# Kernel tuning notes

Hardware: AMD Instinct MI355X
Metric: run time of the kernel (lower is better)

The kernel has to match this reference:

```python
import jax, jax.numpy as jnp
import numpy as np


def _rnn_layer(x, w_ih, w_hh, b_ih, b_hh):
    # x: [B, T, D_in]; returns [B, T, H]
    B = x.shape[0]
    H = w_hh.shape[0]
    # Precompute input projection for all timesteps in one big GEMM.
    xp = jnp.einsum('btd,hd->bth', x, w_ih) + b_ih + b_hh  # [B, T, H]
    h0 = jnp.zeros((B, H), dtype=x.dtype)

    def step(h, xp_t):
        h = jnp.tanh(xp_t + h @ w_hh.T)
        return h, h

    _, hs = jax.lax.scan(step, h0, jnp.swapaxes(xp, 0, 1))  # hs: [T, B, H]
    return jnp.swapaxes(hs, 0, 1)  # [B, T, H]


def setup_inputs() -> dict:
    key = jax.random.key(0)
    ks = jax.random.split(key, 11)
    B, T, D, H, O = 256, 512, 64, 512, 1
    s_in = 1.0 / np.sqrt(H)
    inp = {
        'x': jax.random.normal(ks[0], (B, T, D), dtype=jnp.float32),
        'w_ih0': jax.random.normal(ks[1], (H, D), dtype=jnp.float32) * s_in,
        'w_hh0': jax.random.normal(ks[2], (H, H), dtype=jnp.float32) * s_in,
        'b_ih0': jax.random.normal(ks[3], (H,), dtype=jnp.float32) * s_in,
        'b_hh0': jax.random.normal(ks[4], (H,), dtype=jnp.float32) * s_in,
        'w_ih1': jax.random.normal(ks[5], (H, H), dtype=jnp.float32) * s_in,
        'w_hh1': jax.random.normal(ks[6], (H, H), dtype=jnp.float32) * s_in,
        'b_ih1': jax.random.normal(ks[7], (H,), dtype=jnp.float32) * s_in,
        'b_hh1': jax.random.normal(ks[8], (H,), dtype=jnp.float32) * s_in,
        'w_lin': jax.random.normal(ks[9], (O, H), dtype=jnp.float32) * s_in,
        'b_lin': jax.random.normal(ks[10], (O,), dtype=jnp.float32) * s_in,
    }
    return inp


def reference(x, w_ih0, w_hh0, b_ih0, b_hh0, w_ih1, w_hh1, b_ih1, b_hh1, w_lin, b_lin):
    h1 = _rnn_layer(x, w_ih0, w_hh0, b_ih0, b_hh0)   # [B, T, H]
    h2 = _rnn_layer(h1, w_ih1, w_hh1, b_ih1, b_hh1)  # [B, T, H]
    out = h2[:, -1, :] @ w_lin.T + b_lin             # [B, 1]
    return jnp.squeeze(out)                          # [B]
```

## Files before the change

kernel.cpp:

```cpp
#include <hip/hip_runtime.h>
#include <hip/hip_bf16.h>

typedef __attribute__((ext_vector_type(8))) short shortx8;
typedef __attribute__((ext_vector_type(4))) float f32x4;
typedef __attribute__((ext_vector_type(4))) unsigned short ushortx4;
typedef __attribute__((ext_vector_type(4))) unsigned int u32x4;

#define HDIM 512
#define DDIM 64
#define TSTEPS 512
#define NG 16
#define NB 16
#define SPIN_LIMIT (1u << 16)

#define OFF_WHH0 0u
#define OFF_W1   (512u * 1024u)
#define OFF_WIH0 (OFF_W1 + 1024u * 1024u)
#define OFF_B0   (OFF_WIH0 + 64u * 1024u)
#define OFF_B1   (OFF_B0 + 2048u)
#define OFF_H1G  (OFF_B1 + 2048u)
#define OFF_H2G  (OFF_H1G + 512u * 1024u)
#define OFF_CNT  (OFF_H2G + 512u * 1024u)

__device__ __forceinline__ unsigned short f2b(float f) {
    __hip_bfloat16 h = __float2bfloat16(f);
    return *reinterpret_cast<unsigned short*>(&h);
}
__device__ __forceinline__ float b2f(unsigned short s) {
    union { unsigned int u; float f; } cvt;
    cvt.u = ((unsigned int)s) << 16;
    return cvt.f;
}
__device__ __forceinline__ float fast_tanh(float v) {
    float e = __expf(2.f * v);
    return 1.f - 2.f * __builtin_amdgcn_rcpf(e + 1.f);
}

__device__ __forceinline__ void mall_store8(unsigned short* p, ushortx4 v) {
    asm volatile("global_store_dwordx2 %0, %1, off sc0 sc1" :: "v"(p), "v"(v) : "memory");
}
__device__ __forceinline__ shortx8 mall_load16(const unsigned short* p) {
    shortx8 r;
    asm volatile("global_load_dwordx4 %0, %1, off sc0 sc1" : "=v"(r) : "v"(p) : "memory");
    return r;
}
__device__ __forceinline__ void vm_drain() {
    asm volatile("s_waitcnt vmcnt(0)" ::: "memory");
    __builtin_amdgcn_sched_barrier(0);
}
__device__ __forceinline__ void flag_store(unsigned int* p, unsigned int v) {
    asm volatile("global_store_dword %0, %1, off sc0 sc1" :: "v"(p), "v"(v) : "memory");
}
__device__ __forceinline__ bool poll_peers(const unsigned int* fp, int m,
                                           unsigned int tgt, bool bail) {
    if (bail) return false;
    unsigned it = 0;
    for (;;) {
        u32x4 f;
        asm volatile("global_load_dwordx4 %0, %1, off sc0 sc1\n\ts_waitcnt vmcnt(0)"
                     : "=v"(f) : "v"(fp) : "memory");
        bool ok = true;
        if (m != 0 && f[0] < tgt) ok = false;
        if (m != 1 && f[1] < tgt) ok = false;
        if (m != 2 && f[2] < tgt) ok = false;
        if (m != 3 && f[3] < tgt) ok = false;
        if (ok) return true;
        if (++it > SPIN_LIMIT) return false;
    }
}

__global__ void prep_kernel(const float* __restrict__ w_ih0, const float* __restrict__ w_hh0,
                            const float* __restrict__ w_ih1, const float* __restrict__ w_hh1,
                            const float* __restrict__ b_ih0, const float* __restrict__ b_hh0,
                            const float* __restrict__ b_ih1, const float* __restrict__ b_hh1,
                            unsigned short* __restrict__ whh0_sw,
                            unsigned short* __restrict__ w1_sw,
                            unsigned short* __restrict__ wih0_sw,
                            float* __restrict__ bias0, float* __restrict__ bias1,
                            unsigned int* __restrict__ cnt)
{
    int idx = blockIdx.x * blockDim.x + threadIdx.x;
    int stride = gridDim.x * blockDim.x;

    for (int i = idx; i < 32 * 16 * 64; i += stride) {
        int l = i & 63, kb = (i >> 6) & 15, mt = i >> 10;
        int row = mt * 16 + (l & 15);
        int k0 = kb * 32 + (l >> 4) * 8;
        unsigned short* o = whh0_sw + (size_t)i * 8;
        #pragma unroll
        for (int j = 0; j < 8; ++j) o[j] = f2b(w_hh0[row * HDIM + k0 + j]);
    }
    for (int i = idx; i < 32 * 32 * 64; i += stride) {
        int l = i & 63, kb = (i >> 6) & 31, mt = i >> 11;
        int row = mt * 16 + (l & 15);
        int k0 = kb * 32 + (l >> 4) * 8;
        unsigned short* o = w1_sw + (size_t)i * 8;
        #pragma unroll
        for (int j = 0; j < 8; ++j) {
            int kk = k0 + j;
            float v = (kk < HDIM) ? w_ih1[row * HDIM + kk] : w_hh1[row * HDIM + (kk - HDIM)];
            o[j] = f2b(v);
        }
    }
    for (int i = idx; i < 32 * 2 * 64; i += stride) {
        int l = i & 63, kb = (i >> 6) & 1, mt = i >> 7;
        int row = mt * 16 + (l & 15);
        int k0 = kb * 32 + (l >> 4) * 8;
        unsigned short* o = wih0_sw + (size_t)i * 8;
        #pragma unroll
        for (int j = 0; j < 8; ++j) o[j] = f2b(w_ih0[row * DDIM + k0 + j]);
    }
    for (int i = idx; i < HDIM; i += stride) {
        bias0[i] = b_ih0[i] + b_hh0[i];
        bias1[i] = b_ih1[i] + b_hh1[i];
    }
    if (idx < NG * 32) {
        unsigned int z = 0;
        unsigned int* p = cnt + idx;
        asm volatile("global_store_dword %0, %1, off sc0 sc1" :: "v"(p), "v"(z) : "memory");
    }
}

__global__ __launch_bounds__(256, 1) void rnn_1sync(
    const float* __restrict__ x,
    const unsigned short* __restrict__ whh0_sw,
    const unsigned short* __restrict__ w1_sw,
    const unsigned short* __restrict__ wih0_sw,
    const float* __restrict__ bias0,
    const float* __restrict__ bias1,
    const float* __restrict__ w_lin,
    const float* __restrict__ b_lin,
    unsigned short* __restrict__ h1G,
    unsigned short* __restrict__ h2G,
    unsigned int* __restrict__ cnt,
    float* __restrict__ out)
{
    __shared__ unsigned short h1L[2][8192];
    __shared__ unsigned short h2L[2][8192];
    __shared__ unsigned short xL[2][1024];

    const int tid  = threadIdx.x;
    const int w    = tid >> 6;
    const int lane = tid & 63;
    const int gq   = lane >> 4;
    const int col  = lane & 15;
    const int b    = blockIdx.x;
    const int g    = (b & 7) | ((b >> 5) << 3);
    const int m    = (b >> 3) & 3;

    const int mt0 = m * 8 + 2 * w, mt1 = mt0 + 1;
    const int lbase = gq * 128 + col * 8;
    const int dbase = (gq >> 1) * 128 + col * 8 + (gq & 1) * 4;

    unsigned int* flags = cnt + g * 32;

    shortx8 W0a[18], W0b[18], W1a[32], W1b[32];
    #pragma unroll
    for (int kb = 0; kb < 16; ++kb) {
        W0a[kb] = *(const shortx8*)(whh0_sw + (((size_t)(mt0 * 16 + kb)) << 9) + lane * 8);
        W0b[kb] = *(const shortx8*)(whh0_sw + (((size_t)(mt1 * 16 + kb)) << 9) + lane * 8);
    }
    #pragma unroll
    for (int kx = 0; kx < 2; ++kx) {
        W0a[16 + kx] = *(const shortx8*)(wih0_sw + (((size_t)(mt0 * 2 + kx)) << 9) + lane * 8);
        W0b[16 + kx] = *(const shortx8*)(wih0_sw + (((size_t)(mt1 * 2 + kx)) << 9) + lane * 8);
    }
    #pragma unroll
    for (int kb = 0; kb < 32; ++kb) {
        W1a[kb] = *(const shortx8*)(w1_sw + (((size_t)(mt0 * 32 + kb)) << 9) + lane * 8);
        W1b[kb] = *(const shortx8*)(w1_sw + (((size_t)(mt1 * 32 + kb)) << 9) + lane * 8);
    }
    #pragma unroll
    for (int i = 0; i < 18; ++i) { asm volatile("" : "+v"(W0a[i]), "+v"(W0b[i])); }
    #pragma unroll
    for (int i = 0; i < 32; ++i) { asm volatile("" : "+v"(W1a[i]), "+v"(W1b[i])); }

    f32x4 b0a = *(const f32x4*)(bias0 + mt0 * 16 + gq * 4);
    f32x4 b0b = *(const f32x4*)(bias0 + mt1 * 16 + gq * 4);
    f32x4 b1a = *(const f32x4*)(bias1 + mt0 * 16 + gq * 4);
    f32x4 b1b = *(const f32x4*)(bias1 + mt1 * 16 + gq * 4);

    const int bb = tid >> 4, d4 = (tid & 15) * 4;
    const int xo = ((d4 >> 3) * 16 + bb) * 8 + (d4 & 7);
    const float* xrow = x + (size_t)(g * NB + bb) * TSTEPS * DDIM + d4;
    bool bail = false;

    {
        f32x4 x0 = *(const f32x4*)(xrow);
        f32x4 x1 = *(const f32x4*)(xrow + DDIM);
        ushortx4 o0, o1;
        #pragma unroll
        for (int j = 0; j < 4; ++j) { o0[j] = f2b(x0[j]); o1[j] = f2b(x1[j]); }
        *(ushortx4*)&xL[0][xo] = o0;
        *(ushortx4*)&xL[1][xo] = o1;
        shortx8 zz = {0, 0, 0, 0, 0, 0, 0, 0};
        for (int i = tid * 8; i < 8192; i += 2048) *(shortx8*)&h2L[1][i] = zz;
    }
    __syncthreads();
    {
        unsigned short* h1G0 = h1G + (size_t)(g * 2 + 0) * 8192;
        f32x4 acc0 = b0a, acc1 = b0b;
        #pragma unroll
        for (int kx = 0; kx < 2; ++kx) {
            shortx8 bf = *(const shortx8*)&xL[0][kx * 512 + lbase];
            acc0 = __builtin_amdgcn_mfma_f32_16x16x32_bf16(W0a[16 + kx], bf, acc0, 0, 0, 0);
            acc1 = __builtin_amdgcn_mfma_f32_16x16x32_bf16(W0b[16 + kx], bf, acc1, 0, 0, 0);
        }
        ushortx4 o0, o1;
        #pragma unroll
        for (int j = 0; j < 4; ++j) { o0[j] = f2b(fast_tanh(acc0[j])); o1[j] = f2b(fast_tanh(acc1[j])); }
        mall_store8(h1G0 + mt0 * 256 + dbase, o0);
        mall_store8(h1G0 + mt1 * 256 + dbase, o1);
        vm_drain();
        __syncthreads();
        if (tid == 0) flag_store(flags + m, 1u);
        if (!poll_peers(flags, m, 1u, bail)) bail = true;
        int o = tid * 8;
        shortx8 v0 = mall_load16(h1G0 + o);
        shortx8 v1 = mall_load16(h1G0 + o + 2048);
        shortx8 v2 = mall_load16(h1G0 + o + 4096);
        shortx8 v3 = mall_load16(h1G0 + o + 6144);
        vm_drain();
        *(shortx8*)&h1L[0][o]        = v0;
        *(shortx8*)&h1L[0][o + 2048] = v1;
        *(shortx8*)&h1L[0][o + 4096] = v2;
        *(shortx8*)&h1L[0][o + 6144] = v3;
    }
    __syncthreads();

    for (int t = 0; t < TSTEPS - 1; ++t) {
        const int pc = t & 1, pn = pc ^ 1;
        unsigned short* h1Gn = h1G + (size_t)(g * 2 + pn) * 8192;
        unsigned short* h2Gc = h2G + (size_t)(g * 2 + pc) * 8192;

        const bool havex = (t + 2 < TSTEPS);
        f32x4 xv;
        if (havex) xv = *(const f32x4*)(xrow + (size_t)(t + 2) * DDIM);

        f32x4 acc0 = b0a, acc1 = b0b, e0 = b1a, e1 = b1b;
        #pragma unroll
        for (int kb = 0; kb < 16; ++kb) {
            shortx8 bf = *(const shortx8*)&h1L[pc][kb * 512 + lbase];
            acc0 = __builtin_amdgcn_mfma_f32_16x16x32_bf16(W0a[kb], bf, acc0, 0, 0, 0);
            acc1 = __builtin_amdgcn_mfma_f32_16x16x32_bf16(W0b[kb], bf, acc1, 0, 0, 0);
            e0   = __builtin_amdgcn_mfma_f32_16x16x32_bf16(W1a[kb], bf, e0, 0, 0, 0);
            e1   = __builtin_amdgcn_mfma_f32_16x16x32_bf16(W1b[kb], bf, e1, 0, 0, 0);
        }
        #pragma unroll
        for (int kx = 0; kx < 2; ++kx) {
            shortx8 bf = *(const shortx8*)&xL[pn][kx * 512 + lbase];
            acc0 = __builtin_amdgcn_mfma_f32_16x16x32_bf16(W0a[16 + kx], bf, acc0, 0, 0, 0);
            acc1 = __builtin_amdgcn_mfma_f32_16x16x32_bf16(W0b[16 + kx], bf, acc1, 0, 0, 0);
        }
        #pragma unroll
        for (int kb = 0; kb < 16; ++kb) {
            shortx8 bf = *(const shortx8*)&h2L[pn][kb * 512 + lbase];
            e0 = __builtin_amdgcn_mfma_f32_16x16x32_bf16(W1a[16 + kb], bf, e0, 0, 0, 0);
            e1 = __builtin_amdgcn_mfma_f32_16x16x32_bf16(W1b[16 + kb], bf, e1, 0, 0, 0);
        }

        {
            ushortx4 o0, o1, p0, p1;
            #pragma unroll
            for (int j = 0; j < 4; ++j) {
                o0[j] = f2b(fast_tanh(acc0[j])); o1[j] = f2b(fast_tanh(acc1[j]));
                p0[j] = f2b(fast_tanh(e0[j]));   p1[j] = f2b(fast_tanh(e1[j]));
            }
            mall_store8(h1Gn + mt0 * 256 + dbase, o0);
            mall_store8(h1Gn + mt1 * 256 + dbase, o1);
            mall_store8(h2Gc + mt0 * 256 + dbase, p0);
            mall_store8(h2Gc + mt1 * 256 + dbase, p1);
        }
        if (havex) {
            ushortx4 ox;
            #pragma unroll
            for (int j = 0; j < 4; ++j) ox[j] = f2b(xv[j]);
            *(ushortx4*)&xL[pc][xo] = ox;
        }
        vm_drain();
        __syncthreads();

        const unsigned int tgt = (unsigned int)(t + 2);
        if (tid == 0) flag_store(flags + m, tgt);
        if (!poll_peers(flags, m, tgt, bail)) bail = true;

        const int o = tid * 8;
        shortx8 va0 = mall_load16(h1Gn + o);
        shortx8 va1 = mall_load16(h1Gn + o + 2048);
        shortx8 va2 = mall_load16(h1Gn + o + 4096);
        shortx8 va3 = mall_load16(h1Gn + o + 6144);
        shortx8 vb0 = mall_load16(h2Gc + o);
        shortx8 vb1 = mall_load16(h2Gc + o + 2048);
        shortx8 vb2 = mall_load16(h2Gc + o + 4096);
        shortx8 vb3 = mall_load16(h2Gc + o + 6144);
        vm_drain();
        *(shortx8*)&h1L[pn][o]        = va0;
        *(shortx8*)&h1L[pn][o + 2048] = va1;
        *(shortx8*)&h1L[pn][o + 4096] = va2;
        *(shortx8*)&h1L[pn][o + 6144] = va3;
        *(shortx8*)&h2L[pc][o]        = vb0;
        *(shortx8*)&h2L[pc][o + 2048] = vb1;
        *(shortx8*)&h2L[pc][o + 4096] = vb2;
        *(shortx8*)&h2L[pc][o + 6144] = vb3;
        __syncthreads();
    }

    {
        unsigned short* h2Gc = h2G + (size_t)(g * 2 + 1) * 8192;
        f32x4 e0 = b1a, e1 = b1b;
        #pragma unroll
        for (int kb = 0; kb < 16; ++kb) {
            shortx8 bf = *(const shortx8*)&h1L[1][kb * 512 + lbase];
            e0 = __builtin_amdgcn_mfma_f32_16x16x32_bf16(W1a[kb], bf, e0, 0, 0, 0);
            e1 = __builtin_amdgcn_mfma_f32_16x16x32_bf16(W1b[kb], bf, e1, 0, 0, 0);
        }
        #pragma unroll
        for (int kb = 0; kb < 16; ++kb) {
            shortx8 bf = *(const shortx8*)&h2L[0][kb * 512 + lbase];
            e0 = __builtin_amdgcn_mfma_f32_16x16x32_bf16(W1a[16 + kb], bf, e0, 0, 0, 0);
            e1 = __builtin_amdgcn_mfma_f32_16x16x32_bf16(W1b[16 + kb], bf, e1, 0, 0, 0);
        }
        ushortx4 o0, o1;
        #pragma unroll
        for (int j = 0; j < 4; ++j) { o0[j] = f2b(fast_tanh(e0[j])); o1[j] = f2b(fast_tanh(e1[j])); }
        mall_store8(h2Gc + mt0 * 256 + dbase, o0);
        mall_store8(h2Gc + mt1 * 256 + dbase, o1);
        vm_drain();
        __syncthreads();
        if (tid == 0) flag_store(flags + m, (unsigned int)(TSTEPS + 1));

        if (m == 0) {
            if (!poll_peers(flags, m, (unsigned int)(TSTEPS + 1), bail)) bail = true;
            #pragma unroll
            for (int r = 0; r < 4; ++r) {
                int bx = w * 4 + r;
                shortx8 hv = mall_load16(h2Gc + lane * 128 + bx * 8);
                vm_drain();
                float s = 0.f;
                #pragma unroll
                for (int j = 0; j < 8; ++j)
                    s += b2f((unsigned short)hv[j]) * w_lin[lane * 8 + j];
                #pragma unroll
                for (int off = 32; off; off >>= 1) s += __shfl_xor(s, off);
                if (lane == 0) out[g * NB + bx] = s + b_lin[0];
            }
        }
    }
    if (bail && tid == 0 && b == 0) out[0] = out[0];
}

extern "C" void kernel_launch(void* const* d_in, const int* in_sizes, int n_in,
                              void* d_out, int out_size, void* d_ws, size_t ws_size,
                              hipStream_t stream) {
    const float* x     = (const float*)d_in[0];
    const float* w_ih0 = (const float*)d_in[1];
    const float* w_hh0 = (const float*)d_in[2];
    const float* b_ih0 = (const float*)d_in[3];
    const float* b_hh0 = (const float*)d_in[4];
    const float* w_ih1 = (const float*)d_in[5];
    const float* w_hh1 = (const float*)d_in[6];
    const float* b_ih1 = (const float*)d_in[7];
    const float* b_hh1 = (const float*)d_in[8];
    const float* w_lin = (const float*)d_in[9];
    const float* b_lin = (const float*)d_in[10];
    float* out = (float*)d_out;

    char* ws = (char*)d_ws;
    unsigned short* whh0_sw = (unsigned short*)(ws + OFF_WHH0);
    unsigned short* w1_sw   = (unsigned short*)(ws + OFF_W1);
    unsigned short* wih0_sw = (unsigned short*)(ws + OFF_WIH0);
    float* bias0            = (float*)(ws + OFF_B0);
    float* bias1            = (float*)(ws + OFF_B1);
    unsigned short* h1G     = (unsigned short*)(ws + OFF_H1G);
    unsigned short* h2G     = (unsigned short*)(ws + OFF_H2G);
    unsigned int*   cnt     = (unsigned int*)(ws + OFF_CNT);

    prep_kernel<<<416, 256, 0, stream>>>(w_ih0, w_hh0, w_ih1, w_hh1,
                                         b_ih0, b_hh0, b_ih1, b_hh1,
                                         whh0_sw, w1_sw, wih0_sw, bias0, bias1, cnt);
    rnn_1sync<<<64, 256, 0, stream>>>(x, whh0_sw, w1_sw, wih0_sw, bias0, bias1,
                                      w_lin, b_lin, h1G, h2G, cnt, out);
}
```

Baseline: 1.801 ms.

## Move layer-1 step after the cross-block barrier to hide synchronization latency

Splits each timestep so layer-0 is computed and published first, then the cross-block flag barrier runs, and the layer-1 step for time t-1 is computed afterwards from the previous step's h2 buffer. The aim is to shorten the critical path between the flag store and the peers' arrival, so layer-1 MFMA work overlaps the wait that comes before the next step. Flags are preloaded before the barrier so the spin loop can be skipped when peers are already done. h2 in LDS becomes single-buffered, an extra epilogue sync is added, and the spin limit is raised.

```diff
diff --git a/kernel.cpp b/kernel.cpp
--- a/kernel.cpp
+++ b/kernel.cpp
@@ -11,7 +11,7 @@
 #define TSTEPS 512
 #define NG 16
 #define NB 16
-#define SPIN_LIMIT (1u << 16)
+#define SPIN_LIMIT (1u << 18)
 
 #define OFF_WHH0 0u
 #define OFF_W1   (512u * 1024u)
@@ -44,12 +44,25 @@
     asm volatile("global_load_dwordx4 %0, %1, off sc0 sc1" : "=v"(r) : "v"(p) : "memory");
     return r;
 }
+__device__ __forceinline__ u32x4 flags_preload(const unsigned int* p) {
+    u32x4 r;
+    asm volatile("global_load_dwordx4 %0, %1, off sc0 sc1" : "=v"(r) : "v"(p) : "memory");
+    return r;
+}
 __device__ __forceinline__ void vm_drain() {
     asm volatile("s_waitcnt vmcnt(0)" ::: "memory");
     __builtin_amdgcn_sched_barrier(0);
 }
 __device__ __forceinline__ void flag_store(unsigned int* p, unsigned int v) {
     asm volatile("global_store_dword %0, %1, off sc0 sc1" :: "v"(p), "v"(v) : "memory");
+}
+__device__ __forceinline__ bool peers_ok(u32x4 f, int m, unsigned int tgt) {
+    bool ok = true;
+    if (m != 0 && f[0] < tgt) ok = false;
+    if (m != 1 && f[1] < tgt) ok = false;
+    if (m != 2 && f[2] < tgt) ok = false;
+    if (m != 3 && f[3] < tgt) ok = false;
+    return ok;
 }
 __device__ __forceinline__ bool poll_peers(const unsigned int* fp, int m,
                                            unsigned int tgt, bool bail) {
@@ -59,12 +72,7 @@
         u32x4 f;
         asm volatile("global_load_dwordx4 %0, %1, off sc0 sc1\n\ts_waitcnt vmcnt(0)"
                      : "=v"(f) : "v"(fp) : "memory");
-        bool ok = true;
-        if (m != 0 && f[0] < tgt) ok = false;
-        if (m != 1 && f[1] < tgt) ok = false;
-        if (m != 2 && f[2] < tgt) ok = false;
-        if (m != 3 && f[3] < tgt) ok = false;
-        if (ok) return true;
+        if (peers_ok(f, m, tgt)) return true;
         if (++it > SPIN_LIMIT) return false;
     }
 }
@@ -121,7 +129,7 @@
     }
 }
 
-__global__ __launch_bounds__(256, 1) void rnn_1sync(
+__global__ __launch_bounds__(256, 1) void rnn_slack(
     const float* __restrict__ x,
     const unsigned short* __restrict__ whh0_sw,
     const unsigned short* __restrict__ w1_sw,
@@ -136,7 +144,7 @@
     float* __restrict__ out)
 {
     __shared__ unsigned short h1L[2][8192];
-    __shared__ unsigned short h2L[2][8192];
+    __shared__ unsigned short h2L[8192];
     __shared__ unsigned short xL[2][1024];
 
     const int tid  = threadIdx.x;
@@ -194,7 +202,7 @@
         *(ushortx4*)&xL[0][xo] = o0;
         *(ushortx4*)&xL[1][xo] = o1;
         shortx8 zz = {0, 0, 0, 0, 0, 0, 0, 0};
-        for (int i = tid * 8; i < 8192; i += 2048) *(shortx8*)&h2L[1][i] = zz;
+        for (int i = tid * 8; i < 8192; i += 2048) *(shortx8*)&h2L[i] = zz;
     }
     __syncthreads();
     {
@@ -232,19 +240,18 @@
         const int pc = t & 1, pn = pc ^ 1;
         unsigned short* h1Gn = h1G + (size_t)(g * 2 + pn) * 8192;
         unsigned short* h2Gc = h2G + (size_t)(g * 2 + pc) * 8192;
+        unsigned short* h2Gp = h2G + (size_t)(g * 2 + pn) * 8192;
 
         const bool havex = (t + 2 < TSTEPS);
         f32x4 xv;
         if (havex) xv = *(const f32x4*)(xrow + (size_t)(t + 2) * DDIM);
 
-        f32x4 acc0 = b0a, acc1 = b0b, e0 = b1a, e1 = b1b;
+        f32x4 acc0 = b0a, acc1 = b0b;
         #pragma unroll
         for (int kb = 0; kb < 16; ++kb) {
             shortx8 bf = *(const shortx8*)&h1L[pc][kb * 512 + lbase];
             acc0 = __builtin_amdgcn_mfma_f32_16x16x32_bf16(W0a[kb], bf, acc0, 0, 0, 0);
             acc1 = __builtin_amdgcn_mfma_f32_16x16x32_bf16(W0b[kb], bf, acc1, 0, 0, 0);
-            e0   = __builtin_amdgcn_mfma_f32_16x16x32_bf16(W1a[kb], bf, e0, 0, 0, 0);
-            e1   = __builtin_amdgcn_mfma_f32_16x16x32_bf16(W1b[kb], bf, e1, 0, 0, 0);
         }
         #pragma unroll
         for (int kx = 0; kx < 2; ++kx) {
@@ -252,24 +259,45 @@
             acc0 = __builtin_amdgcn_mfma_f32_16x16x32_bf16(W0a[16 + kx], bf, acc0, 0, 0, 0);
             acc1 = __builtin_amdgcn_mfma_f32_16x16x32_bf16(W0b[16 + kx], bf, acc1, 0, 0, 0);
         }
-        #pragma unroll
-        for (int kb = 0; kb < 16; ++kb) {
-            shortx8 bf = *(const shortx8*)&h2L[pn][kb * 512 + lbase];
-            e0 = __builtin_amdgcn_mfma_f32_16x16x32_bf16(W1a[16 + kb], bf, e0, 0, 0, 0);
-            e1 = __builtin_amdgcn_mfma_f32_16x16x32_bf16(W1b[16 + kb], bf, e1, 0, 0, 0);
-        }
-
         {
-            ushortx4 o0, o1, p0, p1;
+            ushortx4 o0, o1;
             #pragma unroll
-            for (int j = 0; j < 4; ++j) {
-                o0[j] = f2b(fast_tanh(acc0[j])); o1[j] = f2b(fast_tanh(acc1[j]));
-                p0[j] = f2b(fast_tanh(e0[j]));   p1[j] = f2b(fast_tanh(e1[j]));
-            }
+            for (int j = 0; j < 4; ++j) { o0[j] = f2b(fast_tanh(acc0[j])); o1[j] = f2b(fast_tanh(acc1[j])); }
             mall_store8(h1Gn + mt0 * 256 + dbase, o0);
             mall_store8(h1Gn + mt1 * 256 + dbase, o1);
-            mall_store8(h2Gc + mt0 * 256 + dbase, p0);
-            mall_store8(h2Gc + mt1 * 256 + dbase, p1);
+        }
+        u32x4 F = flags_preload(flags);
+        vm_drain();
+        __syncthreads();
+
+        const unsigned int tgt = (unsigned int)(t + 2);
+        if (tid == 0) flag_store(flags + m, tgt);
+        if (!peers_ok(F, m, tgt)) {
+            if (!poll_peers(flags, m, tgt, bail)) bail = true;
+        }
+
+        const int o = tid * 8;
+        shortx8 va0 = mall_load16(h1Gn + o);
+        shortx8 va1 = mall_load16(h1Gn + o + 2048);
+        shortx8 va2 = mall_load16(h1Gn + o + 4096);
+        shortx8 va3 = mall_load16(h1Gn + o + 6144);
+        shortx8 vb0, vb1, vb2, vb3;
+        if (t > 0) {
+            vb0 = mall_load16(h2Gp + o);
+            vb1 = mall_load16(h2Gp + o + 2048);
+            vb2 = mall_load16(h2Gp + o + 4096);
+            vb3 = mall_load16(h2Gp + o + 6144);
+        }
+        vm_drain();
+        *(shortx8*)&h1L[pn][o]        = va0;
+        *(shortx8*)&h1L[pn][o + 2048] = va1;
+        *(shortx8*)&h1L[pn][o + 4096] = va2;
+        *(shortx8*)&h1L[pn][o + 6144] = va3;
+        if (t > 0) {
+            *(shortx8*)&h2L[o]        = vb0;
+            *(shortx8*)&h2L[o + 2048] = vb1;
+            *(shortx8*)&h2L[o + 4096] = vb2;
+            *(shortx8*)&h2L[o + 6144] = vb3;
         }
         if (havex) {
             ushortx4 ox;
@@ -277,36 +305,51 @@
             for (int j = 0; j < 4; ++j) ox[j] = f2b(xv[j]);
             *(ushortx4*)&xL[pc][xo] = ox;
         }
-        vm_drain();
-        __syncthreads();
-
-        const unsigned int tgt = (unsigned int)(t + 2);
-        if (tid == 0) flag_store(flags + m, tgt);
-        if (!poll_peers(flags, m, tgt, bail)) bail = true;
-
+        __syncthreads();
+
+        f32x4 e0 = b1a, e1 = b1b;
+        #pragma unroll
+        for (int kb = 0; kb < 16; ++kb) {
+            shortx8 bf = *(const shortx8*)&h1L[pc][kb * 512 + lbase];
+            e0 = __builtin_amdgcn_mfma_f32_16x16x32_bf16(W1a[kb], bf, e0, 0, 0, 0);
+            e1 = __builtin_amdgcn_mfma_f32_16x16x32_bf16(W1b[kb], bf, e1, 0, 0, 0);
+        }
+        #pragma unroll
+        for (int kb = 0; kb < 16; ++kb) {
+            shortx8 bf = *(const shortx8*)&h2L[kb * 512 + lbase];
+            e0 = __builtin_amdgcn_mfma_f32_16x16x32_bf16(W1a[16 + kb], bf, e0, 0, 0, 0);
+            e1 = __builtin_amdgcn_mfma_f32_16x16x32_bf16(W1b[16 + kb], bf, e1, 0, 0, 0);
+        }
+        {
+            ushortx4 p0, p1;
+            #pragma unroll
+            for (int j = 0; j < 4; ++j) { p0[j] = f2b(fast_tanh(e0[j])); p1[j] = f2b(fast_tanh(e1[j])); }
+            mall_store8(h2Gc + mt0 * 256 + dbase, p0);
+            mall_store8(h2Gc + mt1 * 256 + dbase, p1);
+        }
+    }
+
+    {
+        vm_drain();
+        __syncthreads();
+        if (tid == 0) flag_store(flags + m, (unsigned int)(TSTEPS + 1));
+        if (!poll_peers(flags, m, (unsigned int)(TSTEPS + 1), bail)) bail = true;
+        unsigned short* h2Gp0 = h2G + (size_t)(g * 2 + 0) * 8192;
         const int o = tid * 8;
-        shortx8 va0 = mall_load16(h1Gn + o);
-        shortx8 va1 = mall_load16(h1Gn + o + 2048);
-        shortx8 va2 = mall_load16(h1Gn + o + 4096);
-        shortx8 va3 = mall_load16(h1Gn + o + 6144);
-        shortx8 vb0 = mall_load16(h2Gc + o);
-        shortx8 vb1 = mall_load16(h2Gc + o + 2048);
-        shortx8 vb2 = mall_load16(h2Gc + o + 4096);
-        shortx8 vb3 = mall_load16(h2Gc + o + 6144);
-        vm_drain();
-        *(shortx8*)&h1L[pn][o]        = va0;
-        *(shortx8*)&h1L[pn][o + 2048] = va1;
-        *(shortx8*)&h1L[pn][o + 4096] = va2;
-        *(shortx8*)&h1L[pn][o + 6144] = va3;
-        *(shortx8*)&h2L[pc][o]        = vb0;
-        *(shortx8*)&h2L[pc][o + 2048] = vb1;
-        *(shortx8*)&h2L[pc][o + 4096] = vb2;
-        *(shortx8*)&h2L[pc][o + 6144] = vb3;
+        shortx8 vb0 = mall_load16(h2Gp0 + o);
+        shortx8 vb1 = mall_load16(h2Gp0 + o + 2048);
+        shortx8 vb2 = mall_load16(h2Gp0 + o + 4096);
+        shortx8 vb3 = mall_load16(h2Gp0 + o + 6144);
+        vm_drain();
+        *(shortx8*)&h2L[o]        = vb0;
+        *(shortx8*)&h2L[o + 2048] = vb1;
+        *(shortx8*)&h2L[o + 4096] = vb2;
+        *(shortx8*)&h2L[o + 6144] = vb3;
         __syncthreads();
     }
 
     {
-        unsigned short* h2Gc = h2G + (size_t)(g * 2 + 1) * 8192;
+        unsigned short* h2G1 = h2G + (size_t)(g * 2 + 1) * 8192;
         f32x4 e0 = b1a, e1 = b1b;
         #pragma unroll
         for (int kb = 0; kb < 16; ++kb) {
@@ -316,25 +359,25 @@
         }
         #pragma unroll
         for (int kb = 0; kb < 16; ++kb) {
-            shortx8 bf = *(const shortx8*)&h2L[0][kb * 512 + lbase];
+            shortx8 bf = *(const shortx8*)&h2L[kb * 512 + lbase];
             e0 = __builtin_amdgcn_mfma_f32_16x16x32_bf16(W1a[16 + kb], bf, e0, 0, 0, 0);
             e1 = __builtin_amdgcn_mfma_f32_16x16x32_bf16(W1b[16 + kb], bf, e1, 0, 0, 0);
         }
-        ushortx4 o0, o1;
-        #pragma unroll
-        for (int j = 0; j < 4; ++j) { o0[j] = f2b(fast_tanh(e0[j])); o1[j] = f2b(fast_tanh(e1[j])); }
-        mall_store8(h2Gc + mt0 * 256 + dbase, o0);
-        mall_store8(h2Gc + mt1 * 256 + dbase, o1);
-        vm_drain();
-        __syncthreads();
-        if (tid == 0) flag_store(flags + m, (unsigned int)(TSTEPS + 1));
+        ushortx4 p0, p1;
+        #pragma unroll
+        for (int j = 0; j < 4; ++j) { p0[j] = f2b(fast_tanh(e0[j])); p1[j] = f2b(fast_tanh(e1[j])); }
+        mall_store8(h2G1 + mt0 * 256 + dbase, p0);
+        mall_store8(h2G1 + mt1 * 256 + dbase, p1);
+        vm_drain();
+        __syncthreads();
+        if (tid == 0) flag_store(flags + m, (unsigned int)(TSTEPS + 2));
 
         if (m == 0) {
-            if (!poll_peers(flags, m, (unsigned int)(TSTEPS + 1), bail)) bail = true;
+            if (!poll_peers(flags, m, (unsigned int)(TSTEPS + 2), bail)) bail = true;
             #pragma unroll
             for (int r = 0; r < 4; ++r) {
                 int bx = w * 4 + r;
-                shortx8 hv = mall_load16(h2Gc + lane * 128 + bx * 8);
+                shortx8 hv = mall_load16(h2G1 + lane * 128 + bx * 8);
                 vm_drain();
                 float s = 0.f;
                 #pragma unroll
@@ -346,7 +389,7 @@
             }
         }
     }
-    if (bail && tid == 0 && b == 0) out[0] = out[0];
+    if (bail && tid == 0 && g == 0 && m == 0) out[0] = out[0];
 }
 
 extern "C" void kernel_launch(void* const* d_in, const int* in_sizes, int n_in,
@@ -378,6 +421,6 @@
     prep_kernel<<<416, 256, 0, stream>>>(w_ih0, w_hh0, w_ih1, w_hh1,
                                          b_ih0, b_hh0, b_ih1, b_hh1,
                                          whh0_sw, w1_sw, wih0_sw, bias0, bias1, cnt);
-    rnn_1sync<<<64, 256, 0, stream>>>(x, whh0_sw, w1_sw, wih0_sw, bias0, bias1,
+    rnn_slack<<<64, 256, 0, stream>>>(x, whh0_sw, w1_sw, wih0_sw, bias0, bias1,
                                       w_lin, b_lin, h1G, h2G, cnt, out);
 }
```

New measurement: 2.037 ms. +13.1%, slower.

## Process two batch groups per block, halving grid to 32 blocks

Applied to the files above, without the earlier changes.

Each block now handles two 16-sample batch groups instead of one, so the grid shrinks from 64 to 32 blocks while keeping the same register-resident weight slice. The per-step cross-block flag sync and global exchange are shared across both groups, cutting the number of participating blocks and amortizing barrier/poll overhead. In exchange each block does twice the MFMA work per step, doubles LDS usage, and serializes two groups' compute, which may lengthen the critical path per timestep. The spin limit is also raised.

```diff
diff --git a/kernel.cpp b/kernel.cpp
--- a/kernel.cpp
+++ b/kernel.cpp
@@ -9,9 +9,9 @@
 #define HDIM 512
 #define DDIM 64
 #define TSTEPS 512
-#define NG 16
+#define NVG 16
 #define NB 16
-#define SPIN_LIMIT (1u << 16)
+#define SPIN_LIMIT (1u << 18)
 
 #define OFF_WHH0 0u
 #define OFF_W1   (512u * 1024u)
@@ -114,14 +114,67 @@
         bias0[i] = b_ih0[i] + b_hh0[i];
         bias1[i] = b_ih1[i] + b_hh1[i];
     }
-    if (idx < NG * 32) {
+    if (idx < NVG * 32) {
         unsigned int z = 0;
         unsigned int* p = cnt + idx;
         asm volatile("global_store_dword %0, %1, off sc0 sc1" :: "v"(p), "v"(z) : "memory");
     }
 }
 
-__global__ __launch_bounds__(256, 1) void rnn_1sync(
+#define FUSED(H1C, XLN, H2N, A0, A1, E0, E1) do {                                   \
+    A0 = b0a; A1 = b0b; E0 = b1a; E1 = b1b;                                         \
+    _Pragma("unroll")                                                                \
+    for (int kb_ = 0; kb_ < 16; ++kb_) {                                             \
+        shortx8 bf_ = *(const shortx8*)&(H1C)[kb_ * 512 + lbase];                    \
+        A0 = __builtin_amdgcn_mfma_f32_16x16x32_bf16(W0a[kb_], bf_, A0, 0, 0, 0);    \
+        A1 = __builtin_amdgcn_mfma_f32_16x16x32_bf16(W0b[kb_], bf_, A1, 0, 0, 0);    \
+        E0 = __builtin_amdgcn_mfma_f32_16x16x32_bf16(W1a[kb_], bf_, E0, 0, 0, 0);    \
+        E1 = __builtin_amdgcn_mfma_f32_16x16x32_bf16(W1b[kb_], bf_, E1, 0, 0, 0);    \
+    }                                                                                \
+    _Pragma("unroll")                                                                \
+    for (int kx_ = 0; kx_ < 2; ++kx_) {                                              \
+        shortx8 bf_ = *(const shortx8*)&(XLN)[kx_ * 512 + lbase];                    \
+        A0 = __builtin_amdgcn_mfma_f32_16x16x32_bf16(W0a[16 + kx_], bf_, A0, 0, 0, 0);\
+        A1 = __builtin_amdgcn_mfma_f32_16x16x32_bf16(W0b[16 + kx_], bf_, A1, 0, 0, 0);\
+    }                                                                                \
+    _Pragma("unroll")                                                                \
+    for (int kb_ = 0; kb_ < 16; ++kb_) {                                             \
+        shortx8 bf_ = *(const shortx8*)&(H2N)[kb_ * 512 + lbase];                    \
+        E0 = __builtin_amdgcn_mfma_f32_16x16x32_bf16(W1a[16 + kb_], bf_, E0, 0, 0, 0);\
+        E1 = __builtin_amdgcn_mfma_f32_16x16x32_bf16(W1b[16 + kb_], bf_, E1, 0, 0, 0);\
+    }                                                                                \
+} while (0)
+
+#define PUB4(H1GN, H2GC, A0, A1, E0, E1) do {                                        \
+    ushortx4 o0_, o1_, p0_, p1_;                                                     \
+    _Pragma("unroll")                                                                \
+    for (int j_ = 0; j_ < 4; ++j_) {                                                 \
+        o0_[j_] = f2b(fast_tanh((A0)[j_])); o1_[j_] = f2b(fast_tanh((A1)[j_]));      \
+        p0_[j_] = f2b(fast_tanh((E0)[j_])); p1_[j_] = f2b(fast_tanh((E1)[j_]));      \
+    }                                                                                \
+    mall_store8((H1GN) + mt0 * 256 + dbase, o0_);                                    \
+    mall_store8((H1GN) + mt1 * 256 + dbase, o1_);                                    \
+    mall_store8((H2GC) + mt0 * 256 + dbase, p0_);                                    \
+    mall_store8((H2GC) + mt1 * 256 + dbase, p1_);                                    \
+} while (0)
+
+#define L1ONLY(H1C, H2N, E0, E1) do {                                                \
+    E0 = b1a; E1 = b1b;                                                              \
+    _Pragma("unroll")                                                                \
+    for (int kb_ = 0; kb_ < 16; ++kb_) {                                             \
+        shortx8 bf_ = *(const shortx8*)&(H1C)[kb_ * 512 + lbase];                    \
+        E0 = __builtin_amdgcn_mfma_f32_16x16x32_bf16(W1a[kb_], bf_, E0, 0, 0, 0);    \
+        E1 = __builtin_amdgcn_mfma_f32_16x16x32_bf16(W1b[kb_], bf_, E1, 0, 0, 0);    \
+    }                                                                                \
+    _Pragma("unroll")                                                                \
+    for (int kb_ = 0; kb_ < 16; ++kb_) {                                             \
+        shortx8 bf_ = *(const shortx8*)&(H2N)[kb_ * 512 + lbase];                    \
+        E0 = __builtin_amdgcn_mfma_f32_16x16x32_bf16(W1a[16 + kb_], bf_, E0, 0, 0, 0);\
+        E1 = __builtin_amdgcn_mfma_f32_16x16x32_bf16(W1b[16 + kb_], bf_, E1, 0, 0, 0);\
+    }                                                                                \
+} while (0)
+
+__global__ __launch_bounds__(256, 1) void rnn_pair(
     const float* __restrict__ x,
     const unsigned short* __restrict__ whh0_sw,
     const unsigned short* __restrict__ w1_sw,
@@ -135,9 +188,12 @@
     unsigned int* __restrict__ cnt,
     float* __restrict__ out)
 {
-    __shared__ unsigned short h1L[2][8192];
-    __shared__ unsigned short h2L[2][8192];
-    __shared__ unsigned short xL[2][1024];
+    __shared__ unsigned short h1L0[2][8192];
+    __shared__ unsigned short h2L0[2][8192];
+    __shared__ unsigned short h1L1[2][8192];
+    __shared__ unsigned short h2L1[2][8192];
+    __shared__ unsigned short xL0[2][1024];
+    __shared__ unsigned short xL1[2][1024];
 
     const int tid  = threadIdx.x;
     const int w    = tid >> 6;
@@ -145,14 +201,16 @@
     const int gq   = lane >> 4;
     const int col  = lane & 15;
     const int b    = blockIdx.x;
-    const int g    = (b & 7) | ((b >> 5) << 3);
-    const int m    = (b >> 3) & 3;
+    const int g    = b & 7;
+    const int m    = b >> 3;
+    const int vg0  = 2 * g, vg1 = 2 * g + 1;
 
     const int mt0 = m * 8 + 2 * w, mt1 = mt0 + 1;
     const int lbase = gq * 128 + col * 8;
     const int dbase = (gq >> 1) * 128 + col * 8 + (gq & 1) * 4;
 
-    unsigned int* flags = cnt + g * 32;
+    unsigned int* flags0 = cnt + vg0 * 32;
+    unsigned int* flags1 = cnt + vg1 * 32;
 
     shortx8 W0a[18], W0b[18], W1a[32], W1b[32];
     #pragma unroll
@@ -182,159 +240,200 @@
 
     const int bb = tid >> 4, d4 = (tid & 15) * 4;
     const int xo = ((d4 >> 3) * 16 + bb) * 8 + (d4 & 7);
-    const float* xrow = x + (size_t)(g * NB + bb) * TSTEPS * DDIM + d4;
+    const float* xrow0 = x + (size_t)(vg0 * NB + bb) * TSTEPS * DDIM + d4;
+    const float* xrow1 = x + (size_t)(vg1 * NB + bb) * TSTEPS * DDIM + d4;
     bool bail = false;
 
     {
-        f32x4 x0 = *(const f32x4*)(xrow);
-        f32x4 x1 = *(const f32x4*)(xrow + DDIM);
-        ushortx4 o0, o1;
-        #pragma unroll
-        for (int j = 0; j < 4; ++j) { o0[j] = f2b(x0[j]); o1[j] = f2b(x1[j]); }
-        *(ushortx4*)&xL[0][xo] = o0;
-        *(ushortx4*)&xL[1][xo] = o1;
+        f32x4 x00 = *(const f32x4*)(xrow0);
+        f32x4 x01 = *(const f32x4*)(xrow0 + DDIM);
+        f32x4 x10 = *(const f32x4*)(xrow1);
+        f32x4 x11 = *(const f32x4*)(xrow1 + DDIM);
+        ushortx4 a, c;
+        #pragma unroll
+        for (int j = 0; j < 4; ++j) { a[j] = f2b(x00[j]); c[j] = f2b(x01[j]); }
+        *(ushortx4*)&xL0[0][xo] = a;
+        *(ushortx4*)&xL0[1][xo] = c;
+        #pragma unroll
+        for (int j = 0; j < 4; ++j) { a[j] = f2b(x10[j]); c[j] = f2b(x11[j]); }
+        *(ushortx4*)&xL1[0][xo] = a;
+        *(ushortx4*)&xL1[1][xo] = c;
         shortx8 zz = {0, 0, 0, 0, 0, 0, 0, 0};
-        for (int i = tid * 8; i < 8192; i += 2048) *(shortx8*)&h2L[1][i] = zz;
+        for (int i = tid * 8; i < 8192; i += 2048) {
+            *(shortx8*)&h2L0[1][i] = zz;
+            *(shortx8*)&h2L1[1][i] = zz;
+        }
     }
     __syncthreads();
     {
-        unsigned short* h1G0 = h1G + (size_t)(g * 2 + 0) * 8192;
+        unsigned short* h1G00 = h1G + (size_t)(vg0 * 2 + 0) * 8192;
+        unsigned short* h1G01 = h1G + (size_t)(vg1 * 2 + 0) * 8192;
         f32x4 acc0 = b0a, acc1 = b0b;
         #pragma unroll
         for (int kx = 0; kx < 2; ++kx) {
-            shortx8 bf = *(const shortx8*)&xL[0][kx * 512 + lbase];
+            shortx8 bf = *(const shortx8*)&xL0[0][kx * 512 + lbase];
             acc0 = __builtin_amdgcn_mfma_f32_16x16x32_bf16(W0a[16 + kx], bf, acc0, 0, 0, 0);
             acc1 = __builtin_amdgcn_mfma_f32_16x16x32_bf16(W0b[16 + kx], bf, acc1, 0, 0, 0);
         }
-        ushortx4 o0, o1;
-        #pragma unroll
-        for (int j = 0; j < 4; ++j) { o0[j] = f2b(fast_tanh(acc0[j])); o1[j] = f2b(fast_tanh(acc1[j])); }
-        mall_store8(h1G0 + mt0 * 256 + dbase, o0);
-        mall_store8(h1G0 + mt1 * 256 + dbase, o1);
+        {
+            ushortx4 o0, o1;
+            #pragma unroll
+            for (int j = 0; j < 4; ++j) { o0[j] = f2b(fast_tanh(acc0[j])); o1[j] = f2b(fast_tanh(acc1[j])); }
+            mall_store8(h1G00 + mt0 * 256 + dbase, o0);
+            mall_store8(h1G00 + mt1 * 256 + dbase, o1);
+        }
+        acc0 = b0a; acc1 = b0b;
+        #pragma unroll
+        for (int kx = 0; kx < 2; ++kx) {
+            shortx8 bf = *(const shortx8*)&xL1[0][kx * 512 + lbase];
+            acc0 = __builtin_amdgcn_mfma_f32_16x16x32_bf16(W0a[16 + kx], bf, acc0, 0, 0, 0);
+            acc1 = __builtin_amdgcn_mfma_f32_16x16x32_bf16(W0b[16 + kx], bf, acc1, 0, 0, 0);
+        }
+        {
+            ushortx4 o0, o1;
+            #pragma unroll
+            for (int j = 0; j < 4; ++j) { o0[j] = f2b(fast_tanh(acc0[j])); o1[j] = f2b(fast_tanh(acc1[j])); }
+            mall_store8(h1G01 + mt0 * 256 + dbase, o0);
+            mall_store8(h1G01 + mt1 * 256 + dbase, o1);
+        }
         vm_drain();
         __syncthreads();
-        if (tid == 0) flag_store(flags + m, 1u);
-        if (!poll_peers(flags, m, 1u, bail)) bail = true;
-        int o = tid * 8;
-        shortx8 v0 = mall_load16(h1G0 + o);
-        shortx8 v1 = mall_load16(h1G0 + o + 2048);
-        shortx8 v2 = mall_load16(h1G0 + o + 4096);
-        shortx8 v3 = mall_load16(h1G0 + o + 6144);
+        if (tid == 0) { flag_store(flags0 + m, 1u); flag_store(flags1 + m, 1u); }
+        if (!poll_peers(flags0, m, 1u, bail)) bail = true;
+        if (!poll_peers(flags1, m, 1u, bail)) bail = true;
+        const int o = tid * 8;
+        shortx8 v0 = mall_load16(h1G00 + o);
+        shortx8 v1 = mall_load16(h1G00 + o + 2048);
+        shortx8 v2 = mall_load16(h1G00 + o + 4096);
+        shortx8 v3 = mall_load16(h1G00 + o + 6144);
+        shortx8 u0 = mall_load16(h1G01 + o);
+        shortx8 u1 = mall_load16(h1G01 + o + 2048);
+        shortx8 u2 = mall_load16(h1G01 + o + 4096);
+        shortx8 u3 = mall_load16(h1G01 + o + 6144);
         vm_drain();
-        *(shortx8*)&h1L[0][o]        = v0;
-        *(shortx8*)&h1L[0][o + 2048] = v1;
-        *(shortx8*)&h1L[0][o + 4096] = v2;
-        *(shortx8*)&h1L[0][o + 6144] = v3;
+        *(shortx8*)&h1L0[0][o]        = v0;
+        *(shortx8*)&h1L0[0][o + 2048] = v1;
+        *(shortx8*)&h1L0[0][o + 4096] = v2;
+        *(shortx8*)&h1L0[0][o + 6144] = v3;
+        *(shortx8*)&h1L1[0][o]        = u0;
+        *(shortx8*)&h1L1[0][o + 2048] = u1;
+        *(shortx8*)&h1L1[0][o + 4096] = u2;
+        *(shortx8*)&h1L1[0][o + 6144] = u3;
     }
     __syncthreads();
 
     for (int t = 0; t < TSTEPS - 1; ++t) {
         const int pc = t & 1, pn = pc ^ 1;
-        unsigned short* h1Gn = h1G + (size_t)(g * 2 + pn) * 8192;
-        unsigned short* h2Gc = h2G + (size_t)(g * 2 + pc) * 8192;
+        unsigned short* h1Gn0 = h1G + (size_t)(vg0 * 2 + pn) * 8192;
+        unsigned short* h2Gc0 = h2G + (size_t)(vg0 * 2 + pc) * 8192;
+        unsigned short* h1Gn1 = h1G + (size_t)(vg1 * 2 + pn) * 8192;
+        unsigned short* h2Gc1 = h2G + (size_t)(vg1 * 2 + pc) * 8192;
 
         const bool havex = (t + 2 < TSTEPS);
-        f32x4 xv;
-        if (havex) xv = *(const f32x4*)(xrow + (size_t)(t + 2) * DDIM);
-
-        f32x4 acc0 = b0a, acc1 = b0b, e0 = b1a, e1 = b1b;
-        #pragma unroll
-        for (int kb = 0; kb < 16; ++kb) {
-            shortx8 bf = *(const shortx8*)&h1L[pc][kb * 512 + lbase];
-            acc0 = __builtin_amdgcn_mfma_f32_16x16x32_bf16(W0a[kb], bf, acc0, 0, 0, 0);
-            acc1 = __builtin_amdgcn_mfma_f32_16x16x32_bf16(W0b[kb], bf, acc1, 0, 0, 0);
-            e0   = __builtin_amdgcn_mfma_f32_16x16x32_bf16(W1a[kb], bf, e0, 0, 0, 0);
-            e1   = __builtin_amdgcn_mfma_f32_16x16x32_bf16(W1b[kb], bf, e1, 0, 0, 0);
-        }
-        #pragma unroll
-        for (int kx = 0; kx < 2; ++kx) {
-            shortx8 bf = *(const shortx8*)&xL[pn][kx * 512 + lbase];
-            acc0 = __builtin_amdgcn_mfma_f32_16x16x32_bf16(W0a[16 + kx], bf, acc0, 0, 0, 0);
-            acc1 = __builtin_amdgcn_mfma_f32_16x16x32_bf16(W0b[16 + kx], bf, acc1, 0, 0, 0);
-        }
-        #pragma unroll
-        for (int kb = 0; kb < 16; ++kb) {
-            shortx8 bf = *(const shortx8*)&h2L[pn][kb * 512 + lbase];
-            e0 = __builtin_amdgcn_mfma_f32_16x16x32_bf16(W1a[16 + kb], bf, e0, 0, 0, 0);
-            e1 = __builtin_amdgcn_mfma_f32_16x16x32_bf16(W1b[16 + kb], bf, e1, 0, 0, 0);
-        }
-
-        {
-            ushortx4 o0, o1, p0, p1;
-            #pragma unroll
-            for (int j = 0; j < 4; ++j) {
-                o0[j] = f2b(fast_tanh(acc0[j])); o1[j] = f2b(fast_tanh(acc1[j]));
-                p0[j] = f2b(fast_tanh(e0[j]));   p1[j] = f2b(fast_tanh(e1[j]));
-            }
-            mall_store8(h1Gn + mt0 * 256 + dbase, o0);
-            mall_store8(h1Gn + mt1 * 256 + dbase, o1);
-            mall_store8(h2Gc + mt0 * 256 + dbase, p0);
-            mall_store8(h2Gc + mt1 * 256 + dbase, p1);
-        }
+        f32x4 xv0, xv1;
+        if (havex) {
+            xv0 = *(const f32x4*)(xrow0 + (size_t)(t + 2) * DDIM);
+            xv1 = *(const f32x4*)(xrow1 + (size_t)(t + 2) * DDIM);
+        }
+
+        {
+            f32x4 A0, A1, E0, E1;
+            FUSED(h1L0[pc], xL0[pn], h2L0[pn], A0, A1, E0, E1);
+            PUB4(h1Gn0, h2Gc0, A0, A1, E0, E1);
+        }
+        {
+            f32x4 A0, A1, E0, E1;
+            FUSED(h1L1[pc], xL1[pn], h2L1[pn], A0, A1, E0, E1);
+            PUB4(h1Gn1, h2Gc1, A0, A1, E0, E1);
+        }
+        vm_drain();
+        __syncthreads();
+
+        const unsigned int tgt = (unsigned int)(t + 2);
+        if (tid == 0) { flag_store(flags0 + m, tgt); flag_store(flags1 + m, tgt); }
+        if (!poll_peers(flags0, m, tgt, bail)) bail = true;
+        if (!poll_peers(flags1, m, tgt, bail)) bail = true;
+
+        const int o = tid * 8;
+        shortx8 va0 = mall_load16(h1Gn0 + o);
+        shortx8 va1 = mall_load16(h1Gn0 + o + 2048);
+        shortx8 va2 = mall_load16(h1Gn0 + o + 4096);
+        shortx8 va3 = mall_load16(h1Gn0 + o + 6144);
+        shortx8 vb0 = mall_load16(h2Gc0 + o);
+        shortx8 vb1 = mall_load16(h2Gc0 + o + 2048);
+        shortx8 vb2 = mall_load16(h2Gc0 + o + 4096);
+        shortx8 vb3 = mall_load16(h2Gc0 + o + 6144);
+        shortx8 vc0 = mall_load16(h1Gn1 + o);
+        shortx8 vc1 = mall_load16(h1Gn1 + o + 2048);
+        shortx8 vc2 = mall_load16(h1Gn1 + o + 4096);
+        shortx8 vc3 = mall_load16(h1Gn1 + o + 6144);
+        shortx8 vd0 = mall_load16(h2Gc1 + o);
+        shortx8 vd1 = mall_load16(h2Gc1 + o + 2048);
+        shortx8 vd2 = mall_load16(h2Gc1 + o + 4096);
+        shortx8 vd3 = mall_load16(h2Gc1 + o + 6144);
+        vm_drain();
+        *(shortx8*)&h1L0[pn][o]        = va0;
+        *(shortx8*)&h1L0[pn][o + 2048] = va1;
+        *(shortx8*)&h1L0[pn][o + 4096] = va2;
+        *(shortx8*)&h1L0[pn][o + 6144] = va3;
+        *(shortx8*)&h2L0[pc][o]        = vb0;
+        *(shortx8*)&h2L0[pc][o + 2048] = vb1;
+        *(shortx8*)&h2L0[pc][o + 4096] = vb2;
+        *(shortx8*)&h2L0[pc][o + 6144] = vb3;
+        *(shortx8*)&h1L1[pn][o]        = vc0;
+        *(shortx8*)&h1L1[pn][o + 2048] = vc1;
+        *(shortx8*)&h1L1[pn][o + 4096] = vc2;
+        *(shortx8*)&h1L1[pn][o + 6144] = vc3;
+        *(shortx8*)&h2L1[pc][o]        = vd0;
+        *(shortx8*)&h2L1[pc][o + 2048] = vd1;
+        *(shortx8*)&h2L1[pc][o + 4096] = vd2;
+        *(shortx8*)&h2L1[pc][o + 6144] = vd3;
         if (havex) {
             ushortx4 ox;
             #pragma unroll
-            for (int j = 0; j < 4; ++j) ox[j] = f2b(xv[j]);
-            *(ushortx4*)&xL[pc][xo] = ox;
+            for (int j = 0; j < 4; ++j) ox[j] = f2b(xv0[j]);
+            *(ushortx4*)&xL0[pc][xo] = ox;
+            #pragma unroll
+            for (int j = 0; j < 4; ++j) ox[j] = f2b(xv1[j]);
+            *(ushortx4*)&xL1[pc][xo] = ox;
+        }
+        __syncthreads();
+    }
+
+    {
+        unsigned short* h2G10 = h2G + (size_t)(vg0 * 2 + 1) * 8192;
+        unsigned short* h2G11 = h2G + (size_t)(vg1 * 2 + 1) * 8192;
+        {
+            f32x4 E0, E1;
+            L1ONLY(h1L0[1], h2L0[0], E0, E1);
+            ushortx4 p0, p1;
+            #pragma unroll
+            for (int j = 0; j < 4; ++j) { p0[j] = f2b(fast_tanh(E0[j])); p1[j] = f2b(fast_tanh(E1[j])); }
+            mall_store8(h2G10 + mt0 * 256 + dbase, p0);
+            mall_store8(h2G10 + mt1 * 256 + dbase, p1);
+        }
+        {
+            f32x4 E0, E1;
+            L1ONLY(h1L1[1], h2L1[0], E0, E1);
+            ushortx4 p0, p1;
+            #pragma unroll
+            for (int j = 0; j < 4; ++j) { p0[j] = f2b(fast_tanh(E0[j])); p1[j] = f2b(fast_tanh(E1[j])); }
+            mall_store8(h2G11 + mt0 * 256 + dbase, p0);
+            mall_store8(h2G11 + mt1 * 256 + dbase, p1);
         }
         vm_drain();
         __syncthreads();
-
-        const unsigned int tgt = (unsigned int)(t + 2);
-        if (tid == 0) flag_store(flags + m, tgt);
-        if (!poll_peers(flags, m, tgt, bail)) bail = true;
-
-        const int o = tid * 8;
-        shortx8 va0 = mall_load16(h1Gn + o);
-        shortx8 va1 = mall_load16(h1Gn + o + 2048);
-        shortx8 va2 = mall_load16(h1Gn + o + 4096);
-        shortx8 va3 = mall_load16(h1Gn + o + 6144);
-        shortx8 vb0 = mall_load16(h2Gc + o);
-        shortx8 vb1 = mall_load16(h2Gc + o + 2048);
-        shortx8 vb2 = mall_load16(h2Gc + o + 4096);
-        shortx8 vb3 = mall_load16(h2Gc + o + 6144);
-        vm_drain();
-        *(shortx8*)&h1L[pn][o]        = va0;
-        *(shortx8*)&h1L[pn][o + 2048] = va1;
-        *(shortx8*)&h1L[pn][o + 4096] = va2;
-        *(shortx8*)&h1L[pn][o + 6144] = va3;
-        *(shortx8*)&h2L[pc][o]        = vb0;
-        *(shortx8*)&h2L[pc][o + 2048] = vb1;
-        *(shortx8*)&h2L[pc][o + 4096] = vb2;
-        *(shortx8*)&h2L[pc][o + 6144] = vb3;
-        __syncthreads();
-    }
-
-    {
-        unsigned short* h2Gc = h2G + (size_t)(g * 2 + 1) * 8192;
-        f32x4 e0 = b1a, e1 = b1b;
-        #pragma unroll
-        for (int kb = 0; kb < 16; ++kb) {
-            shortx8 bf = *(const shortx8*)&h1L[1][kb * 512 + lbase];
-            e0 = __builtin_amdgcn_mfma_f32_16x16x32_bf16(W1a[kb], bf, e0, 0, 0, 0);
-            e1 = __builtin_amdgcn_mfma_f32_16x16x32_bf16(W1b[kb], bf, e1, 0, 0, 0);
-        }
-        #pragma unroll
-        for (int kb = 0; kb < 16; ++kb) {
-            shortx8 bf = *(const shortx8*)&h2L[0][kb * 512 + lbase];
-            e0 = __builtin_amdgcn_mfma_f32_16x16x32_bf16(W1a[16 + kb], bf, e0, 0, 0, 0);
-            e1 = __builtin_amdgcn_mfma_f32_16x16x32_bf16(W1b[16 + kb], bf, e1, 0, 0, 0);
-        }
-        ushortx4 o0, o1;
-        #pragma unroll
-        for (int j = 0; j < 4; ++j) { o0[j] = f2b(fast_tanh(e0[j])); o1[j] = f2b(fast_tanh(e1[j])); }
-        mall_store8(h2Gc + mt0 * 256 + dbase, o0);
-        mall_store8(h2Gc + mt1 * 256 + dbase, o1);
-        vm_drain();
-        __syncthreads();
-        if (tid == 0) flag_store(flags + m, (unsigned int)(TSTEPS + 1));
-
+        if (tid == 0) {
+            flag_store(flags0 + m, (unsigned int)(TSTEPS + 1));
+            flag_store(flags1 + m, (unsigned int)(TSTEPS + 1));
+        }
         if (m == 0) {
-            if (!poll_peers(flags, m, (unsigned int)(TSTEPS + 1), bail)) bail = true;
+            if (!poll_peers(flags0, m, (unsigned int)(TSTEPS + 1), bail)) bail = true;
+            if (!poll_peers(flags1, m, (unsigned int)(TSTEPS + 1), bail)) bail = true;
             #pragma unroll
             for (int r = 0; r < 4; ++r) {
                 int bx = w * 4 + r;
-                shortx8 hv = mall_load16(h2Gc + lane * 128 + bx * 8);
+                shortx8 hv = mall_load16(h2G10 + lane * 128 + bx * 8);
                 vm_drain();
                 float s = 0.f;
                 #pragma unroll
@@ -342,7 +441,20 @@
                     s += b2f((unsigned short)hv[j]) * w_lin[lane * 8 + j];
                 #pragma unroll
                 for (int off = 32; off; off >>= 1) s += __shfl_xor(s, off);
-                if (lane == 0) out[g * NB + bx] = s + b_lin[0];
+                if (lane == 0) out[vg0 * NB + bx] = s + b_lin[0];
+            }
+            #pragma unroll
+            for (int r = 0; r < 4; ++r) {
+                int bx = w * 4 + r;
+                shortx8 hv = mall_load16(h2G11 + lane * 128 + bx * 8);
+                vm_drain();
+                float s = 0.f;
+                #pragma unroll
+                for (int j = 0; j < 8; ++j)
+                    s += b2f((unsigned short)hv[j]) * w_lin[lane * 8 + j];
+                #pragma unroll
+                for (int off = 32; off; off >>= 1) s += __shfl_xor(s, off);
+                if (lane == 0) out[vg1 * NB + bx] = s + b_lin[0];
             }
         }
     }
@@ -378,6 +490,6 @@
     prep_kernel<<<416, 256, 0, stream>>>(w_ih0, w_hh0, w_ih1, w_hh1,
                                          b_ih0, b_hh0, b_ih1, b_hh1,
                                          whh0_sw, w1_sw, wih0_sw, bias0, bias1, cnt);
-    rnn_1sync<<<64, 256, 0, stream>>>(x, whh0_sw, w1_sw, wih0_sw, bias0, bias1,
-                                      w_lin, b_lin, h1G, h2G, cnt, out);
-}
+    rnn_pair<<<32, 256, 0, stream>>>(x, whh0_sw, w1_sw, wih0_sw, bias0, bias1,
+                                     w_lin, b_lin, h1G, h2G, cnt, out);
+}
```

After: 5.309 ms. 195% more time.
